# Performance work log

Hardware: AMD Instinct MI355X
Metric: run time of the kernel (lower is better)

Reference implementation:

```python
import jax, jax.numpy as jnp
import numpy as np

B, N, D = 32, 1024, 256

def setup_inputs() -> dict:
    key = jax.random.key(0)
    ks = jax.random.split(key, 7)
    s = 1.0 / np.sqrt(D)
    return {
        "traj": jax.random.normal(ks[0], (B, N, D), dtype=jnp.float32),
        "Wq": jax.random.normal(ks[1], (D, D), dtype=jnp.float32) * s,
        "bq": jax.random.normal(ks[2], (D,), dtype=jnp.float32) * s,
        "Wk": jax.random.normal(ks[3], (D, D), dtype=jnp.float32) * s,
        "bk": jax.random.normal(ks[4], (D,), dtype=jnp.float32) * s,
        "Wv": jax.random.normal(ks[5], (D, D), dtype=jnp.float32) * s,
        "bv": jax.random.normal(ks[6], (D,), dtype=jnp.float32) * s,
    }

def reference(traj, Wq, bq, Wk, bk, Wv, bv):
    # torch nn.Linear: y = x @ W.T + b
    q = jnp.einsum('bnd,ed->bne', traj, Wq) + bq  # [B,N,D]
    k = jnp.einsum('bnd,ed->bne', traj, Wk) + bk  # [B,N,D]
    v = jnp.einsum('bnd,ed->bne', traj, Wv) + bv  # [B,N,D]
    # unscaled dot-product attention (original sums broadcasted Q*K over D)
    scores = jnp.einsum('bnd,bmd->bnm', q, k)     # [B,N,N]
    attn = jax.nn.softmax(scores, axis=-1)        # [B,N,N]
    out = jnp.einsum('bnm,bmd->bnd', attn, v)     # [B,N,D]
    return out
```

## Files before the change

### kernel.cpp

```cpp
#include <hip/hip_runtime.h>

#define NN 1024
#define DD 256

typedef __attribute__((ext_vector_type(8))) _Float16 f16x8;
typedef __attribute__((ext_vector_type(4))) _Float16 f16x4;
typedef __attribute__((ext_vector_type(4))) float f32x4;

union H8 { f16x8 v; _Float16 s[8]; };

__device__ __forceinline__ void g2lds16(const void* g, void* l) {
  __builtin_amdgcn_global_load_lds(
      (const __attribute__((address_space(1))) void*)g,
      (__attribute__((address_space(3))) void*)l, 16, 0, 0);
}

__global__ void wconv_kernel(const float* __restrict__ Wq, const float* __restrict__ Wk,
                             const float* __restrict__ Wv, _Float16* __restrict__ pw) {
  int c = blockIdx.x * 256 + threadIdx.x;
  int lane = c & 63;
  int nt = (c >> 6) & 1;
  int kk = (c >> 7) & 7;
  int et = c >> 10;
  int e = et * 32 + nt * 16 + (lane & 15);
  int d = kk * 32 + (lane >> 4) * 8;
  const float* W = (e < 256) ? Wq : (e < 512 ? Wk : Wv);
  const float* src = W + (e & 255) * 256 + d;
  H8 xx;
  for (int j = 0; j < 8; ++j) xx.s[j] = (_Float16)src[j];
  *(f16x8*)(pw + (size_t)c * 8) = xx.v;
}

__global__ __launch_bounds__(256, 2) void proj_kernel(
    const float* __restrict__ traj,
    const float* __restrict__ bq, const float* __restrict__ bk, const float* __restrict__ bv,
    const _Float16* __restrict__ pw,
    _Float16* __restrict__ pq, _Float16* __restrict__ pk, _Float16* __restrict__ pv)
{
  __shared__ alignas(16) _Float16 Wl[2][8192];
  __shared__ alignas(16) _Float16 Cs[4][1280];

  const int t = threadIdx.x;
  const int lane = t & 63, wave = t >> 6;
  const int col16 = lane & 15, quad = lane >> 4;
  const int mt = blockIdx.x >> 1, eh = blockIdx.x & 1;
  const int mbase = mt * 128;
  const int bb = mbase >> 10;

  f16x8 aq[2][8];
  for (int s = 0; s < 2; ++s) {
    const float* ap = traj + (size_t)(mbase + wave * 32 + s * 16 + col16) * DD;
    for (int kk = 0; kk < 8; ++kk) {
      float4 u0 = *(const float4*)(ap + kk * 32 + quad * 8);
      float4 u1 = *(const float4*)(ap + kk * 32 + quad * 8 + 4);
      H8 xx;
      xx.s[0] = (_Float16)u0.x; xx.s[1] = (_Float16)u0.y;
      xx.s[2] = (_Float16)u0.z; xx.s[3] = (_Float16)u0.w;
      xx.s[4] = (_Float16)u1.x; xx.s[5] = (_Float16)u1.y;
      xx.s[6] = (_Float16)u1.z; xx.s[7] = (_Float16)u1.w;
      aq[s][kk] = xx.v;
    }
  }

  const f32x4 zero = {0.f, 0.f, 0.f, 0.f};
  const int et0 = eh * 12;

  for (int i = 0; i < 4; ++i)
    g2lds16(pw + (size_t)et0 * 8192 + (size_t)(i * 256 + t) * 8, Wl[0] + (i * 256 + t) * 8);

  for (int ei = 0; ei < 12; ++ei) {
    __syncthreads();
    if (ei < 11) {
      const _Float16* ws = pw + (size_t)(et0 + ei + 1) * 8192;
      _Float16* wd = Wl[(ei + 1) & 1];
      for (int i = 0; i < 4; ++i)
        g2lds16(ws + (size_t)(i * 256 + t) * 8, wd + (i * 256 + t) * 8);
    }
    const _Float16* wl = Wl[ei & 1];

    f32x4 acc[2][2];
    acc[0][0] = zero; acc[0][1] = zero; acc[1][0] = zero; acc[1][1] = zero;
    for (int kk = 0; kk < 8; ++kk)
      for (int nt = 0; nt < 2; ++nt) {
        f16x8 bw = *(const f16x8*)&wl[((kk * 2 + nt) * 64 + lane) * 8];
        acc[0][nt] = __builtin_amdgcn_mfma_f32_16x16x32_f16(aq[0][kk], bw, acc[0][nt], 0, 0, 0);
        acc[1][nt] = __builtin_amdgcn_mfma_f32_16x16x32_f16(aq[1][kk], bw, acc[1][nt], 0, 0, 0);
      }

    int e0 = eh * 384 + ei * 32;
    int sel = e0 >> 8;
    const float* bias = (sel == 0) ? bq : (sel == 1 ? bk : bv);
    for (int nt = 0; nt < 2; ++nt) {
      float bvl = bias[(e0 & 255) + nt * 16 + col16];
      for (int s = 0; s < 2; ++s) {
        acc[s][nt][0] += bvl; acc[s][nt][1] += bvl;
        acc[s][nt][2] += bvl; acc[s][nt][3] += bvl;
      }
    }

    _Float16* cs = Cs[wave];
    if (sel < 2) {
      for (int s = 0; s < 2; ++s)
        for (int nt = 0; nt < 2; ++nt)
          for (int r = 0; r < 4; ++r)
            cs[(s * 16 + quad * 4 + r) * 40 + nt * 16 + col16] = (_Float16)acc[s][nt][r];
      if (sel == 0) {
        for (int s = 0; s < 2; ++s) {
          f16x8 val = *(const f16x8*)&cs[(s * 16 + col16) * 40 + quad * 8];
          int g = (mbase >> 4) + wave * 2 + s;
          *(f16x8*)(pq + (size_t)((g * 8 + ei) * 64 + lane) * 8) = val;
        }
      } else {
        int kkg = (e0 - 256) >> 5;
        for (int s = 0; s < 2; ++s) {
          f16x8 val = *(const f16x8*)&cs[(s * 16 + col16) * 40 + quad * 8];
          int kgg = ((mbase & 1023) >> 4) + wave * 2 + s;
          *(f16x8*)(pk + (size_t)(((bb * 64 + kgg) * 8 + kkg) * 64 + lane) * 8) = val;
        }
      }
    } else {
      for (int s = 0; s < 2; ++s)
        for (int nt = 0; nt < 2; ++nt)
          for (int r = 0; r < 4; ++r)
            cs[(nt * 16 + col16) * 40 + s * 16 + quad * 4 + r] = (_Float16)acc[s][nt][r];
      int kt32 = ((mbase & 1023) >> 5) + wave;
      for (int dtl = 0; dtl < 2; ++dtl) {
        const _Float16* base = &cs[(dtl * 16 + col16) * 40];
        H8 val;
        *(f16x4*)&val.s[0] = *(const f16x4*)&base[quad * 4];
        *(f16x4*)&val.s[4] = *(const f16x4*)&base[16 + quad * 4];
        int dtg = ((e0 - 512) >> 4) + dtl;
        *(f16x8*)(pv + (size_t)(((bb * 32 + kt32) * 16 + dtg) * 64 + lane) * 8) = val.v;
      }
    }
  }
}

__global__ __launch_bounds__(256, 2) void attn_kernel(
    const _Float16* __restrict__ pq, const _Float16* __restrict__ pk,
    const _Float16* __restrict__ pv, float* __restrict__ out)
{
  __shared__ alignas(16) _Float16 Ks[2][8192];
  __shared__ alignas(16) _Float16 Vs[2][8192];

  const int t = threadIdx.x;
  const int lane = t & 63, wave = t >> 6;
  const int col16 = lane & 15, quad = lane >> 4;
  const int b = blockIdx.x, qt = blockIdx.y;
  const int qrow0 = b * NN + qt * 64;

  f16x8 aq[8];
  {
    int g = b * 64 + qt * 4 + wave;
#pragma unroll
    for (int kk = 0; kk < 8; ++kk)
      aq[kk] = *(const f16x8*)(pq + (size_t)((g * 8 + kk) * 64 + lane) * 8);
  }

  float m_i = -3.0e38f, l_i = 0.f;
  f32x4 O[16];
  const f32x4 zero = {0.f, 0.f, 0.f, 0.f};
#pragma unroll
  for (int dt = 0; dt < 16; ++dt) O[dt] = zero;

  const _Float16* kbb = pk + (size_t)b * 64 * 8 * 64 * 8;
  const _Float16* vbb = pv + (size_t)b * 32 * 16 * 64 * 8;

#pragma unroll
  for (int i = 0; i < 4; ++i) g2lds16(kbb + (size_t)(i * 256 + t) * 8, &Ks[0][(i * 256 + t) * 8]);
#pragma unroll
  for (int i = 0; i < 4; ++i) g2lds16(vbb + (size_t)(i * 256 + t) * 8, &Vs[0][(i * 256 + t) * 8]);
#pragma unroll
  for (int i = 0; i < 4; ++i) g2lds16(kbb + 8192 + (size_t)(i * 256 + t) * 8, &Ks[1][(i * 256 + t) * 8]);
#pragma unroll
  for (int i = 0; i < 4; ++i) g2lds16(vbb + 8192 + (size_t)(i * 256 + t) * 8, &Vs[1][(i * 256 + t) * 8]);

  for (int kt = 0; kt < 32; ++kt) {
    if (kt < 31) asm volatile("s_waitcnt vmcnt(8)" ::: "memory");
    else         asm volatile("s_waitcnt vmcnt(0)" ::: "memory");
    __builtin_amdgcn_s_barrier();
    asm volatile("" ::: "memory");

    const _Float16* ks = Ks[kt & 1];
    f32x4 S[2]; S[0] = zero; S[1] = zero;
    __builtin_amdgcn_s_setprio(1);
#pragma unroll
    for (int kk = 0; kk < 8; ++kk)
#pragma unroll
      for (int nt = 0; nt < 2; ++nt) {
        f16x8 bk_ = *(const f16x8*)&ks[((nt * 8 + kk) * 64 + lane) * 8];
        S[nt] = __builtin_amdgcn_mfma_f32_16x16x32_f16(bk_, aq[kk], S[nt], 0, 0, 0);
      }
    __builtin_amdgcn_s_setprio(0);

    float sv[8];
#pragma unroll
    for (int nt = 0; nt < 2; ++nt)
#pragma unroll
      for (int r = 0; r < 4; ++r) sv[nt * 4 + r] = S[nt][r];
    float vmax = sv[0];
#pragma unroll
    for (int j = 1; j < 8; ++j) vmax = fmaxf(vmax, sv[j]);
    vmax = fmaxf(vmax, __shfl_xor(vmax, 16));
    vmax = fmaxf(vmax, __shfl_xor(vmax, 32));

    if (__ballot(vmax > m_i + 8.0f)) {
      float nm = fmaxf(m_i, vmax);
      float alpha = __expf(m_i - nm);
      float a4[4];
#pragma unroll
      for (int r = 0; r < 4; ++r) a4[r] = __shfl(alpha, quad * 4 + r);
#pragma unroll
      for (int dt = 0; dt < 16; ++dt)
#pragma unroll
        for (int r = 0; r < 4; ++r) O[dt][r] *= a4[r];
      l_i *= alpha;
      m_i = nm;
    }
    float rs = 0.f;
    H8 px;
#pragma unroll
    for (int j = 0; j < 8; ++j) {
      float pj = __expf(sv[j] - m_i);
      rs += pj;
      px.s[j] = (_Float16)pj;
    }
    rs += __shfl_xor(rs, 16);
    rs += __shfl_xor(rs, 32);
    l_i += rs;
    f16x8 ap = px.v;

    const _Float16* vs = Vs[kt & 1];
    __builtin_amdgcn_s_setprio(1);
#pragma unroll
    for (int dt = 0; dt < 16; ++dt) {
      f16x8 bv_ = *(const f16x8*)&vs[(dt * 64 + lane) * 8];
      O[dt] = __builtin_amdgcn_mfma_f32_16x16x32_f16(ap, bv_, O[dt], 0, 0, 0);
    }
    __builtin_amdgcn_s_setprio(0);

    asm volatile("" ::: "memory");
    __builtin_amdgcn_s_barrier();
    if (kt < 30) {
      const _Float16* kg = kbb + (size_t)(kt + 2) * 8192;
      const _Float16* vg = vbb + (size_t)(kt + 2) * 8192;
      _Float16* kd = Ks[kt & 1];
      _Float16* vd = Vs[kt & 1];
#pragma unroll
      for (int i = 0; i < 4; ++i) g2lds16(kg + (size_t)(i * 256 + t) * 8, kd + (i * 256 + t) * 8);
#pragma unroll
      for (int i = 0; i < 4; ++i) g2lds16(vg + (size_t)(i * 256 + t) * 8, vd + (i * 256 + t) * 8);
    }
  }

  float linv[4];
#pragma unroll
  for (int r = 0; r < 4; ++r) linv[r] = 1.0f / __shfl(l_i, quad * 4 + r);
#pragma unroll
  for (int r = 0; r < 4; ++r) {
    float* orow = out + (size_t)(qrow0 + wave * 16 + quad * 4 + r) * DD;
#pragma unroll
    for (int dt = 0; dt < 16; ++dt)
      orow[dt * 16 + col16] = O[dt][r] * linv[r];
  }
}

extern "C" void kernel_launch(void* const* d_in, const int* in_sizes, int n_in,
                              void* d_out, int out_size, void* d_ws, size_t ws_size,
                              hipStream_t stream) {
  const float* traj = (const float*)d_in[0];
  const float* Wq   = (const float*)d_in[1];
  const float* bq   = (const float*)d_in[2];
  const float* Wk   = (const float*)d_in[3];
  const float* bk   = (const float*)d_in[4];
  const float* Wv   = (const float*)d_in[5];
  const float* bv   = (const float*)d_in[6];

  _Float16* pq = (_Float16*)d_ws;
  _Float16* pk = pq + (size_t)32768 * 256;
  _Float16* pv = pk + (size_t)32768 * 256;
  _Float16* pw = pv + (size_t)32768 * 256;

  wconv_kernel<<<96, 256, 0, stream>>>(Wq, Wk, Wv, pw);
  proj_kernel<<<512, 256, 0, stream>>>(traj, bq, bk, bv, pw, pq, pk, pv);
  attn_kernel<<<dim3(32, 16), 256, 0, stream>>>(pq, pk, pv, (float*)d_out);
}
```

Before: 164.2 us.

## Process two query sub-tiles per wave to reuse K/V LDS fragments

```diff
diff --git a/kernel.cpp b/kernel.cpp
--- a/kernel.cpp
+++ b/kernel.cpp
@@ -136,7 +136,7 @@
   }
 }
 
-__global__ __launch_bounds__(256, 2) void attn_kernel(
+__global__ __launch_bounds__(128, 1) void attn_kernel(
     const _Float16* __restrict__ pq, const _Float16* __restrict__ pk,
     const _Float16* __restrict__ pv, float* __restrict__ out)
 {
@@ -149,93 +149,104 @@
   const int b = blockIdx.x, qt = blockIdx.y;
   const int qrow0 = b * NN + qt * 64;
 
-  f16x8 aq[8];
-  {
-    int g = b * 64 + qt * 4 + wave;
+  f16x8 aq[2][8];
+#pragma unroll
+  for (int s = 0; s < 2; ++s) {
+    int g = b * 64 + qt * 4 + wave * 2 + s;
 #pragma unroll
     for (int kk = 0; kk < 8; ++kk)
-      aq[kk] = *(const f16x8*)(pq + (size_t)((g * 8 + kk) * 64 + lane) * 8);
-  }
-
-  float m_i = -3.0e38f, l_i = 0.f;
-  f32x4 O[16];
+      aq[s][kk] = *(const f16x8*)(pq + (size_t)((g * 8 + kk) * 64 + lane) * 8);
+  }
+
+  float m_i[2] = {-3.0e38f, -3.0e38f};
+  float l_i[2] = {0.f, 0.f};
+  f32x4 O[2][16];
   const f32x4 zero = {0.f, 0.f, 0.f, 0.f};
 #pragma unroll
-  for (int dt = 0; dt < 16; ++dt) O[dt] = zero;
+  for (int s = 0; s < 2; ++s)
+#pragma unroll
+    for (int dt = 0; dt < 16; ++dt) O[s][dt] = zero;
 
   const _Float16* kbb = pk + (size_t)b * 64 * 8 * 64 * 8;
   const _Float16* vbb = pv + (size_t)b * 32 * 16 * 64 * 8;
 
 #pragma unroll
-  for (int i = 0; i < 4; ++i) g2lds16(kbb + (size_t)(i * 256 + t) * 8, &Ks[0][(i * 256 + t) * 8]);
-#pragma unroll
-  for (int i = 0; i < 4; ++i) g2lds16(vbb + (size_t)(i * 256 + t) * 8, &Vs[0][(i * 256 + t) * 8]);
-#pragma unroll
-  for (int i = 0; i < 4; ++i) g2lds16(kbb + 8192 + (size_t)(i * 256 + t) * 8, &Ks[1][(i * 256 + t) * 8]);
-#pragma unroll
-  for (int i = 0; i < 4; ++i) g2lds16(vbb + 8192 + (size_t)(i * 256 + t) * 8, &Vs[1][(i * 256 + t) * 8]);
+  for (int i = 0; i < 8; ++i) g2lds16(kbb + (size_t)(i * 128 + t) * 8, &Ks[0][(i * 128 + t) * 8]);
+#pragma unroll
+  for (int i = 0; i < 8; ++i) g2lds16(vbb + (size_t)(i * 128 + t) * 8, &Vs[0][(i * 128 + t) * 8]);
+#pragma unroll
+  for (int i = 0; i < 8; ++i) g2lds16(kbb + 8192 + (size_t)(i * 128 + t) * 8, &Ks[1][(i * 128 + t) * 8]);
+#pragma unroll
+  for (int i = 0; i < 8; ++i) g2lds16(vbb + 8192 + (size_t)(i * 128 + t) * 8, &Vs[1][(i * 128 + t) * 8]);
 
   for (int kt = 0; kt < 32; ++kt) {
-    if (kt < 31) asm volatile("s_waitcnt vmcnt(8)" ::: "memory");
+    if (kt < 31) asm volatile("s_waitcnt vmcnt(16)" ::: "memory");
     else         asm volatile("s_waitcnt vmcnt(0)" ::: "memory");
     __builtin_amdgcn_s_barrier();
     asm volatile("" ::: "memory");
 
     const _Float16* ks = Ks[kt & 1];
-    f32x4 S[2]; S[0] = zero; S[1] = zero;
+    f32x4 S[2][2];
+    S[0][0] = zero; S[0][1] = zero; S[1][0] = zero; S[1][1] = zero;
     __builtin_amdgcn_s_setprio(1);
 #pragma unroll
     for (int kk = 0; kk < 8; ++kk)
 #pragma unroll
       for (int nt = 0; nt < 2; ++nt) {
         f16x8 bk_ = *(const f16x8*)&ks[((nt * 8 + kk) * 64 + lane) * 8];
-        S[nt] = __builtin_amdgcn_mfma_f32_16x16x32_f16(bk_, aq[kk], S[nt], 0, 0, 0);
+        S[0][nt] = __builtin_amdgcn_mfma_f32_16x16x32_f16(bk_, aq[0][kk], S[0][nt], 0, 0, 0);
+        S[1][nt] = __builtin_amdgcn_mfma_f32_16x16x32_f16(bk_, aq[1][kk], S[1][nt], 0, 0, 0);
       }
     __builtin_amdgcn_s_setprio(0);
 
-    float sv[8];
-#pragma unroll
-    for (int nt = 0; nt < 2; ++nt)
-#pragma unroll
-      for (int r = 0; r < 4; ++r) sv[nt * 4 + r] = S[nt][r];
-    float vmax = sv[0];
-#pragma unroll
-    for (int j = 1; j < 8; ++j) vmax = fmaxf(vmax, sv[j]);
-    vmax = fmaxf(vmax, __shfl_xor(vmax, 16));
-    vmax = fmaxf(vmax, __shfl_xor(vmax, 32));
-
-    if (__ballot(vmax > m_i + 8.0f)) {
-      float nm = fmaxf(m_i, vmax);
-      float alpha = __expf(m_i - nm);
-      float a4[4];
-#pragma unroll
-      for (int r = 0; r < 4; ++r) a4[r] = __shfl(alpha, quad * 4 + r);
-#pragma unroll
-      for (int dt = 0; dt < 16; ++dt)
-#pragma unroll
-        for (int r = 0; r < 4; ++r) O[dt][r] *= a4[r];
-      l_i *= alpha;
-      m_i = nm;
-    }
-    float rs = 0.f;
-    H8 px;
-#pragma unroll
-    for (int j = 0; j < 8; ++j) {
-      float pj = __expf(sv[j] - m_i);
-      rs += pj;
-      px.s[j] = (_Float16)pj;
-    }
-    rs += __shfl_xor(rs, 16);
-    rs += __shfl_xor(rs, 32);
-    l_i += rs;
-    f16x8 ap = px.v;
+    f16x8 ap[2];
+#pragma unroll
+    for (int s = 0; s < 2; ++s) {
+      float sv[8];
+#pragma unroll
+      for (int nt = 0; nt < 2; ++nt)
+#pragma unroll
+        for (int r = 0; r < 4; ++r) sv[nt * 4 + r] = S[s][nt][r];
+      float vmax = sv[0];
+#pragma unroll
+      for (int j = 1; j < 8; ++j) vmax = fmaxf(vmax, sv[j]);
+      vmax = fmaxf(vmax, __shfl_xor(vmax, 16));
+      vmax = fmaxf(vmax, __shfl_xor(vmax, 32));
+
+      if (__ballot(vmax > m_i[s] + 8.0f)) {
+        float nm = fmaxf(m_i[s], vmax);
+        float alpha = __expf(m_i[s] - nm);
+        float a4[4];
+#pragma unroll
+        for (int r = 0; r < 4; ++r) a4[r] = __shfl(alpha, quad * 4 + r);
+#pragma unroll
+        for (int dt = 0; dt < 16; ++dt)
+#pragma unroll
+          for (int r = 0; r < 4; ++r) O[s][dt][r] *= a4[r];
+        l_i[s] *= alpha;
+        m_i[s] = nm;
+      }
+      float rs = 0.f;
+      H8 px;
+#pragma unroll
+      for (int j = 0; j < 8; ++j) {
+        float pj = __expf(sv[j] - m_i[s]);
+        rs += pj;
+        px.s[j] = (_Float16)pj;
+      }
+      rs += __shfl_xor(rs, 16);
+      rs += __shfl_xor(rs, 32);
+      l_i[s] += rs;
+      ap[s] = px.v;
+    }
 
     const _Float16* vs = Vs[kt & 1];
     __builtin_amdgcn_s_setprio(1);
 #pragma unroll
     for (int dt = 0; dt < 16; ++dt) {
       f16x8 bv_ = *(const f16x8*)&vs[(dt * 64 + lane) * 8];
-      O[dt] = __builtin_amdgcn_mfma_f32_16x16x32_f16(ap, bv_, O[dt], 0, 0, 0);
+      O[0][dt] = __builtin_amdgcn_mfma_f32_16x16x32_f16(ap[0], bv_, O[0][dt], 0, 0, 0);
+      O[1][dt] = __builtin_amdgcn_mfma_f32_16x16x32_f16(ap[1], bv_, O[1][dt], 0, 0, 0);
     }
     __builtin_amdgcn_s_setprio(0);
 
@@ -247,21 +258,24 @@
       _Float16* kd = Ks[kt & 1];
       _Float16* vd = Vs[kt & 1];
 #pragma unroll
-      for (int i = 0; i < 4; ++i) g2lds16(kg + (size_t)(i * 256 + t) * 8, kd + (i * 256 + t) * 8);
-#pragma unroll
-      for (int i = 0; i < 4; ++i) g2lds16(vg + (size_t)(i * 256 + t) * 8, vd + (i * 256 + t) * 8);
-    }
-  }
-
-  float linv[4];
-#pragma unroll
-  for (int r = 0; r < 4; ++r) linv[r] = 1.0f / __shfl(l_i, quad * 4 + r);
-#pragma unroll
-  for (int r = 0; r < 4; ++r) {
-    float* orow = out + (size_t)(qrow0 + wave * 16 + quad * 4 + r) * DD;
-#pragma unroll
-    for (int dt = 0; dt < 16; ++dt)
-      orow[dt * 16 + col16] = O[dt][r] * linv[r];
+      for (int i = 0; i < 8; ++i) g2lds16(kg + (size_t)(i * 128 + t) * 8, kd + (i * 128 + t) * 8);
+#pragma unroll
+      for (int i = 0; i < 8; ++i) g2lds16(vg + (size_t)(i * 128 + t) * 8, vd + (i * 128 + t) * 8);
+    }
+  }
+
+#pragma unroll
+  for (int s = 0; s < 2; ++s) {
+    float linv[4];
+#pragma unroll
+    for (int r = 0; r < 4; ++r) linv[r] = 1.0f / __shfl(l_i[s], quad * 4 + r);
+#pragma unroll
+    for (int r = 0; r < 4; ++r) {
+      float* orow = out + (size_t)(qrow0 + wave * 32 + s * 16 + quad * 4 + r) * DD;
+#pragma unroll
+      for (int dt = 0; dt < 16; ++dt)
+        orow[dt * 16 + col16] = O[s][dt][r] * linv[r];
+    }
   }
 }
 
@@ -283,5 +297,5 @@
 
   wconv_kernel<<<96, 256, 0, stream>>>(Wq, Wk, Wv, pw);
   proj_kernel<<<512, 256, 0, stream>>>(traj, bq, bk, bv, pw, pq, pk, pv);
-  attn_kernel<<<dim3(32, 16), 256, 0, stream>>>(pq, pk, pv, (float*)d_out);
-}
+  attn_kernel<<<dim3(32, 16), 128, 0, stream>>>(pq, pk, pv, (float*)d_out);
+}
```

Result: slower. 183.6 us (+11.8%).
